# Kernel optimization log

Measured on AMD Instinct MI355X. Metric: run time of the kernel, lower is better.

The kernel has to match this reference:

```python
import jax, jax.numpy as jnp
import numpy as np

B, T, A, FA = 4, 1024, 8, 16   # batch, frames, animals, per-animal feat
C, H, L = 1024, 16, 8          # n_embd, n_head, n_layer
D_IN, D_OUT = A * FA, 256


def _ln(x, g, b, eps=1e-5):
    mu = x.mean(-1, keepdims=True)
    var = ((x - mu) ** 2).mean(-1, keepdims=True)
    return (x - mu) * jax.lax.rsqrt(var + eps) * g + b


def setup_inputs() -> dict:
    key = jax.random.key(0)
    ks = iter(jax.random.split(key, 32))
    w = lambda shape: jax.random.normal(next(ks), shape, jnp.float32) * 0.02
    inp = {
        'tokens': jax.random.normal(next(ks), (B, T, A, FA), jnp.float32),
        'tok_emb_w': w((D_IN, C)), 'tok_emb_b': jnp.zeros((C,), jnp.float32),
        # per-layer params stacked along leading n_layer axis
        'ln1_g': jnp.ones((L, C), jnp.float32), 'ln1_b': jnp.zeros((L, C), jnp.float32),
        'Wq': w((L, C, C)), 'bq': jnp.zeros((L, C), jnp.float32),
        'Wk': w((L, C, C)), 'bk': jnp.zeros((L, C), jnp.float32),
        'Wv': w((L, C, C)), 'bv': jnp.zeros((L, C), jnp.float32),
        'Wo': w((L, C, C)), 'bo': jnp.zeros((L, C), jnp.float32),
        'ln2_g': jnp.ones((L, C), jnp.float32), 'ln2_b': jnp.zeros((L, C), jnp.float32),
        'W1': w((L, C, 4 * C)), 'b1': jnp.zeros((L, 4 * C), jnp.float32),
        'W2': w((L, 4 * C, C)), 'b2': jnp.zeros((L, C), jnp.float32),
        'lnf_g': jnp.ones((C,), jnp.float32), 'lnf_b': jnp.zeros((C,), jnp.float32),
        'proj_w': w((C, D_OUT)), 'proj_b': jnp.zeros((D_OUT,), jnp.float32),
        'dec_w1': w((D_OUT, D_OUT)), 'dec_b1': jnp.zeros((D_OUT,), jnp.float32),
        'dec_ln_g': jnp.ones((D_OUT,), jnp.float32), 'dec_ln_b': jnp.zeros((D_OUT,), jnp.float32),
        'dec_w2': w((D_OUT, D_IN)), 'dec_b2': jnp.zeros((D_IN,), jnp.float32),
    }
    return inp


def reference(tokens, tok_emb_w, tok_emb_b, ln1_g, ln1_b, Wq, bq, Wk, bk, Wv, bv,
              Wo, bo, ln2_g, ln2_b, W1, b1, W2, b2, lnf_g, lnf_b, proj_w, proj_b,
              dec_w1, dec_b1, dec_ln_g, dec_ln_b, dec_w2, dec_b2):
    b, t = tokens.shape[0], tokens.shape[1]
    x = tokens.reshape(b, t, -1)                      # (B,T,D_IN) flatten(2)
    h = x @ tok_emb_w + tok_emb_b                     # (B,T,C)
    mask = jnp.tril(jnp.ones((t, t), bool))           # causal mask
    dh = C // H
    scale = 1.0 / np.sqrt(dh)

    def layer(h, p):
        g1, bb1, wq, bq_, wk, bk_, wv, bv_, wo, bo_, g2, bb2, w1, b1_, w2, b2_ = p
        a = _ln(h, g1, bb1)
        q = (a @ wq + bq_).reshape(b, t, H, dh).transpose(0, 2, 1, 3)
        k = (a @ wk + bk_).reshape(b, t, H, dh).transpose(0, 2, 1, 3)
        v = (a @ wv + bv_).reshape(b, t, H, dh).transpose(0, 2, 1, 3)
        att = jnp.einsum('bhqd,bhkd->bhqk', q, k) * scale
        att = jnp.where(mask, att, -jnp.inf)
        att = jax.nn.softmax(att, axis=-1)
        y = jnp.einsum('bhqk,bhkd->bhqd', att, v)
        y = y.transpose(0, 2, 1, 3).reshape(b, t, C)
        h = h + (y @ wo + bo_)
        m = _ln(h, g2, bb2)
        h = h + jax.nn.gelu(m @ w1 + b1_, approximate=False) @ w2 + b2_
        return h, None

    h, _ = jax.lax.scan(layer, h, (ln1_g, ln1_b, Wq, bq, Wk, bk, Wv, bv, Wo, bo,
                                   ln2_g, ln2_b, W1, b1, W2, b2))
    feats = _ln(h, lnf_g, lnf_b) @ proj_w + proj_b    # (B,T,D_OUT)
    # decode=True path: decoder_frame then frame-delta prediction
    pred = _ln(jnp.tanh(feats @ dec_w1 + dec_b1), dec_ln_g, dec_ln_b) @ dec_w2 + dec_b2
    return pred[:, :-1] - x[:, 1:]                    # (B,T-1,D_IN)
```

## Files before the change

kernel.cpp:

```cpp
#include <hip/hip_runtime.h>
#include <hip/hip_bf16.h>

typedef unsigned short u16;
typedef __attribute__((ext_vector_type(8))) short bf16x8;
typedef __attribute__((ext_vector_type(4))) float f32x4;

#define BT     4096
#define CDIM   1024
#define NH     16
#define FF     4096
#define DIN    128
#define DOUT   256
#define NLAYER 8
#define TSEQ   1024
#define NBATCH 4

__device__ inline u16 f2bfu(float v) {
    __hip_bfloat16 h = __float2bfloat16(v);
    return __builtin_bit_cast(unsigned short, h);
}

__device__ inline void async_copy16(const u16* g, u16* l) {
    __builtin_amdgcn_global_load_lds((const __attribute__((address_space(1))) void*)g,
                                     (__attribute__((address_space(3))) void*)l,
                                     16, 0, 0);
}

template<int ACT, int RES, int OBF, int EPI>
__global__ __launch_bounds__(256) void gemm_bt(
    const u16* __restrict__ A, const u16* __restrict__ Bt,
    const float* __restrict__ bias, const float* res,
    void* outp, u16* __restrict__ vtp, int N, int K, int Kc)
{
    __shared__ __align__(16) u16 As[128 * 32];
    __shared__ __align__(16) u16 Bs[128 * 32];
    int tid  = threadIdx.x;
    int wave = tid >> 6, lane = tid & 63;
    int ln = lane & 15, quad = lane >> 4;
    int wm = (wave >> 1) * 64, wn = (wave & 1) * 64;
    int k0 = blockIdx.z * Kc;
    const u16* Ab = A  + (size_t)blockIdx.y * 128 * K;
    const u16* Bb = Bt + (size_t)blockIdx.x * 128 * K;
    f32x4 acc[4][4] = {};
    for (int kt = k0; kt < k0 + Kc; kt += 32) {
#pragma unroll
        for (int it = 0; it < 2; ++it) {
            int e = it * 256 + tid;
            int row = e >> 2, col = (e & 3) * 8;
            int lbase = (it * 256 + wave * 64) * 8;
            async_copy16(Ab + (size_t)row * K + kt + col, As + lbase);
            async_copy16(Bb + (size_t)row * K + kt + col, Bs + lbase);
        }
        __syncthreads();
        bf16x8 af[4], bfr[4];
#pragma unroll
        for (int i = 0; i < 4; ++i)
            af[i] = *(const bf16x8*)&As[(wm + i * 16 + ln) * 32 + quad * 8];
#pragma unroll
        for (int j = 0; j < 4; ++j)
            bfr[j] = *(const bf16x8*)&Bs[(wn + j * 16 + ln) * 32 + quad * 8];
#pragma unroll
        for (int i = 0; i < 4; ++i)
#pragma unroll
            for (int j = 0; j < 4; ++j)
                acc[i][j] = __builtin_amdgcn_mfma_f32_16x16x32_bf16(af[i], bfr[j], acc[i][j], 0, 0, 0);
        __syncthreads();
    }
    int gr0 = blockIdx.y * 128 + wm + quad * 4;
    int gc0 = blockIdx.x * 128 + wn + ln;
#pragma unroll
    for (int i = 0; i < 4; ++i) {
#pragma unroll
        for (int j = 0; j < 4; ++j) {
            int gc = gc0 + j * 16;
            float bv = (EPI == 1) ? ((blockIdx.z == 0) ? bias[gc] : 0.0f) : bias[gc];
#pragma unroll
            for (int r = 0; r < 4; ++r) {
                int gr = gr0 + i * 16 + r;
                float v = acc[i][j][r] + bv;
                if (ACT == 1) v = 0.5f * v * (1.0f + erff(v * 0.70710678118654752f));
                if (ACT == 2) v = tanhf(v);
                if (EPI == 1) {
                    unsafeAtomicAdd(&((float*)outp)[(size_t)gr * N + gc], v);
                } else if (EPI == 2) {
                    if ((int)blockIdx.x < 16) {
                        ((u16*)outp)[(size_t)gr * 2048 + gc] = f2bfu(v);
                    } else {
                        int c2 = gc - 2048;
                        int hh = c2 >> 6, f = c2 & 63;
                        int bb = gr >> 10, t = gr & 1023;
                        vtp[((size_t)(bb * 16 + hh) * 64 + f) * TSEQ + t] = f2bfu(v);
                    }
                } else {
                    size_t idx = (size_t)gr * N + gc;
                    if (RES) v += res[idx];
                    if (OBF) ((u16*)outp)[idx] = f2bfu(v);
                    else     ((float*)outp)[idx] = v;
                }
            }
        }
    }
}

__global__ __launch_bounds__(64) void attn_kernel(const u16* __restrict__ qk,
    const u16* __restrict__ vT, u16* __restrict__ y)
{
    __shared__ __align__(16) u16 Plds[2][16 * 32];
    int qt = blockIdx.x, bh = blockIdx.y;
    int b = bh >> 4, h = bh & 15;
    int q0 = qt * 32;
    int lane = threadIdx.x;
    int ln = lane & 15, quad = lane >> 4;
    const u16* qbase = qk + (size_t)b * TSEQ * 2048;
    bf16x8 qf[2][2];
#pragma unroll
    for (int qi = 0; qi < 2; ++qi) {
        const u16* qrow = qbase + (size_t)(q0 + qi * 16 + ln) * 2048 + h * 64 + quad * 8;
        qf[qi][0] = *(const bf16x8*)qrow;
        qf[qi][1] = *(const bf16x8*)(qrow + 32);
    }
    const u16* vbase = vT + (size_t)bh * 64 * TSEQ;
    f32x4 O[2][4] = {};
    float m_i[2][4], l_i[2][4];
#pragma unroll
    for (int qi = 0; qi < 2; ++qi)
#pragma unroll
        for (int r = 0; r < 4; ++r) { m_i[qi][r] = -1e30f; l_i[qi][r] = 0.0f; }
    int nkt = qt + 1;
    for (int kt = 0; kt < nkt; ++kt) {
        int j0 = kt * 32;
        bf16x8 kf[2][2];
#pragma unroll
        for (int kk = 0; kk < 2; ++kk) {
            const u16* krow = qbase + (size_t)(j0 + kk * 16 + ln) * 2048 + 1024 + h * 64 + quad * 8;
            kf[kk][0] = *(const bf16x8*)krow;
            kf[kk][1] = *(const bf16x8*)(krow + 32);
        }
        f32x4 S[2][2] = {};
#pragma unroll
        for (int qi = 0; qi < 2; ++qi)
#pragma unroll
            for (int kk = 0; kk < 2; ++kk) {
                S[qi][kk] = __builtin_amdgcn_mfma_f32_16x16x32_bf16(qf[qi][0], kf[kk][0], S[qi][kk], 0, 0, 0);
                S[qi][kk] = __builtin_amdgcn_mfma_f32_16x16x32_bf16(qf[qi][1], kf[kk][1], S[qi][kk], 0, 0, 0);
            }
        bool lastt = (kt == qt);
        float alpha[2][4];
#pragma unroll
        for (int qi = 0; qi < 2; ++qi) {
#pragma unroll
            for (int r = 0; r < 4; ++r) {
                float s0 = S[qi][0][r] * 0.125f, s1 = S[qi][1][r] * 0.125f;
                if (lastt) {
                    int qr = q0 + qi * 16 + quad * 4 + r;
                    if (j0 + ln > qr)      s0 = -1e30f;
                    if (j0 + 16 + ln > qr) s1 = -1e30f;
                }
                float mx = fmaxf(s0, s1);
                mx = fmaxf(mx, __shfl_xor(mx, 1));
                mx = fmaxf(mx, __shfl_xor(mx, 2));
                mx = fmaxf(mx, __shfl_xor(mx, 4));
                mx = fmaxf(mx, __shfl_xor(mx, 8));
                float mn = fmaxf(m_i[qi][r], mx);
                float al = __expf(m_i[qi][r] - mn);
                float p0 = __expf(s0 - mn);
                float p1 = __expf(s1 - mn);
                float rs = p0 + p1;
                rs += __shfl_xor(rs, 1);
                rs += __shfl_xor(rs, 2);
                rs += __shfl_xor(rs, 4);
                rs += __shfl_xor(rs, 8);
                l_i[qi][r] = l_i[qi][r] * al + rs;
                m_i[qi][r] = mn;
                alpha[qi][r] = al;
                Plds[qi][(quad * 4 + r) * 32 + ln]      = f2bfu(p0);
                Plds[qi][(quad * 4 + r) * 32 + 16 + ln] = f2bfu(p1);
            }
#pragma unroll
            for (int nt = 0; nt < 4; ++nt)
#pragma unroll
                for (int r = 0; r < 4; ++r)
                    O[qi][nt][r] *= alpha[qi][r];
        }
        __syncthreads();
        bf16x8 pa0 = *(const bf16x8*)&Plds[0][ln * 32 + quad * 8];
        bf16x8 pa1 = *(const bf16x8*)&Plds[1][ln * 32 + quad * 8];
#pragma unroll
        for (int nt = 0; nt < 4; ++nt) {
            bf16x8 vf = *(const bf16x8*)(vbase + (size_t)(nt * 16 + ln) * TSEQ + j0 + quad * 8);
            O[0][nt] = __builtin_amdgcn_mfma_f32_16x16x32_bf16(pa0, vf, O[0][nt], 0, 0, 0);
            O[1][nt] = __builtin_amdgcn_mfma_f32_16x16x32_bf16(pa1, vf, O[1][nt], 0, 0, 0);
        }
        __syncthreads();
    }
#pragma unroll
    for (int qi = 0; qi < 2; ++qi)
#pragma unroll
        for (int r = 0; r < 4; ++r) {
            float invl = 1.0f / l_i[qi][r];
            int row = q0 + qi * 16 + quad * 4 + r;
#pragma unroll
            for (int nt = 0; nt < 4; ++nt)
                y[(size_t)(b * TSEQ + row) * CDIM + h * 64 + nt * 16 + ln] = f2bfu(O[qi][nt][r] * invl);
        }
}

template<int NPT>
__global__ __launch_bounds__(256) void ln_kernel(const float* __restrict__ x,
    const float* __restrict__ g, const float* __restrict__ bet, u16* __restrict__ out)
{
    const int n = NPT * 256;
    int row = blockIdx.x, tid = threadIdx.x;
    const float* xr = x + (size_t)row * n;
    float xv[NPT];
    float s1 = 0.f, s2 = 0.f;
#pragma unroll
    for (int k = 0; k < NPT; ++k) {
        float v = xr[k * 256 + tid];
        xv[k] = v; s1 += v; s2 += v * v;
    }
#pragma unroll
    for (int m = 1; m < 64; m <<= 1) { s1 += __shfl_xor(s1, m); s2 += __shfl_xor(s2, m); }
    __shared__ float red[8];
    int wv = tid >> 6;
    if ((tid & 63) == 0) { red[wv] = s1; red[4 + wv] = s2; }
    __syncthreads();
    s1 = red[0] + red[1] + red[2] + red[3];
    s2 = red[4] + red[5] + red[6] + red[7];
    float mu = s1 * (1.0f / n);
    float var = s2 * (1.0f / n) - mu * mu;
    float rs = rsqrtf(var + 1e-5f);
#pragma unroll
    for (int k = 0; k < NPT; ++k) {
        int c = k * 256 + tid;
        out[(size_t)row * n + c] = f2bfu((xv[k] - mu) * rs * g[c] + bet[c]);
    }
}

__device__ inline void tile_tc(const float* src, u16* dst, int K, int N, int kt, int nt,
                               int tid, float* sm)
{
    int c = tid & 31, r0 = tid >> 5;
#pragma unroll
    for (int rr = r0; rr < 32; rr += 8)
        sm[rr * 33 + c] = src[(size_t)(kt * 32 + rr) * N + nt * 32 + c];
    __syncthreads();
#pragma unroll
    for (int rr = r0; rr < 32; rr += 8)
        dst[(size_t)(nt * 32 + rr) * K + kt * 32 + c] = f2bfu(sm[c * 33 + rr]);
}

__global__ __launch_bounds__(256) void transpose_cvt(const float* __restrict__ src,
    u16* __restrict__ dst, int K, int N)
{
    __shared__ float sm[32 * 33];
    tile_tc(src, dst, K, N, blockIdx.y, blockIdx.x, threadIdx.x, sm);
}

__global__ __launch_bounds__(256) void prep_layer(
    const float* __restrict__ Wq, const float* __restrict__ Wk, const float* __restrict__ Wv,
    const float* __restrict__ Wo, const float* __restrict__ W1, const float* __restrict__ W2,
    const float* __restrict__ bq, const float* __restrict__ bk, const float* __restrict__ bv,
    u16* __restrict__ qkv_t, u16* __restrict__ wo_t, u16* __restrict__ w1_t,
    u16* __restrict__ w2_t, float* __restrict__ bias3)
{
    __shared__ float sm[32 * 33];
    int id = blockIdx.x, tid = threadIdx.x;
    const float* src; u16* dst; int K, N, kt, nt;
    if (id < 3072) {
        int w = id >> 10, t = id & 1023;
        src = (w == 0) ? Wq : ((w == 1) ? Wk : Wv);
        dst = qkv_t + (size_t)w * CDIM * CDIM;
        K = CDIM; N = CDIM; kt = t >> 5; nt = t & 31;
    } else if (id < 4096) {
        int t = id - 3072; src = Wo; dst = wo_t; K = CDIM; N = CDIM; kt = t >> 5; nt = t & 31;
    } else if (id < 8192) {
        int t = id - 4096; src = W1; dst = w1_t; K = CDIM; N = FF;   kt = t >> 7; nt = t & 127;
    } else {
        int t = id - 8192; src = W2; dst = w2_t; K = FF;   N = CDIM; kt = t >> 5; nt = t & 31;
    }
    tile_tc(src, dst, K, N, kt, nt, tid, sm);
    if (id < 3) {
        const float* bsrc = (id == 0) ? bq : ((id == 1) ? bk : bv);
        for (int k2 = tid; k2 < CDIM; k2 += 256) bias3[id * CDIM + k2] = bsrc[k2];
    }
}

__global__ __launch_bounds__(256) void cvt_bf16(const float* __restrict__ src,
    u16* __restrict__ dst, int n)
{
    int i = blockIdx.x * 256 + threadIdx.x;
    if (i < n) dst[i] = f2bfu(src[i]);
}

__global__ __launch_bounds__(256) void zero_f32(float* __restrict__ dst, int n)
{
    int i = blockIdx.x * 256 + threadIdx.x;
    if (i < n) dst[i] = 0.0f;
}

__global__ __launch_bounds__(256) void out_sub(const float* __restrict__ pred,
    const float* __restrict__ x, float* __restrict__ out, int total)
{
    int i = blockIdx.x * 256 + threadIdx.x;
    if (i >= total) return;
    int b = i / ((TSEQ - 1) * DIN);
    int rtmp = i - b * (TSEQ - 1) * DIN;
    int t = rtmp >> 7, f = rtmp & 127;
    out[i] = pred[(size_t)(b * TSEQ + t) * DIN + f] - x[(size_t)(b * TSEQ + t + 1) * DIN + f];
}

__global__ void fail_flag(float* out) { if (threadIdx.x == 0 && blockIdx.x == 0) out[0] = 1.0e6f; }

extern "C" void kernel_launch(void* const* d_in, const int* in_sizes, int n_in,
                              void* d_out, int out_size, void* d_ws, size_t ws_size,
                              hipStream_t stream)
{
    (void)in_sizes; (void)n_in; (void)out_size;
    const float* tokens    = (const float*)d_in[0];
    const float* tok_emb_w = (const float*)d_in[1];
    const float* tok_emb_b = (const float*)d_in[2];
    const float* ln1_g = (const float*)d_in[3];
    const float* ln1_b = (const float*)d_in[4];
    const float* Wq = (const float*)d_in[5];
    const float* bq = (const float*)d_in[6];
    const float* Wk = (const float*)d_in[7];
    const float* bk = (const float*)d_in[8];
    const float* Wv = (const float*)d_in[9];
    const float* bv = (const float*)d_in[10];
    const float* Wo = (const float*)d_in[11];
    const float* bo = (const float*)d_in[12];
    const float* ln2_g = (const float*)d_in[13];
    const float* ln2_b = (const float*)d_in[14];
    const float* W1 = (const float*)d_in[15];
    const float* b1 = (const float*)d_in[16];
    const float* W2 = (const float*)d_in[17];
    const float* b2 = (const float*)d_in[18];
    const float* lnf_g = (const float*)d_in[19];
    const float* lnf_b = (const float*)d_in[20];
    const float* proj_w = (const float*)d_in[21];
    const float* proj_b = (const float*)d_in[22];
    const float* dec_w1 = (const float*)d_in[23];
    const float* dec_b1 = (const float*)d_in[24];
    const float* dec_ln_g = (const float*)d_in[25];
    const float* dec_ln_b = (const float*)d_in[26];
    const float* dec_w2 = (const float*)d_in[27];
    const float* dec_b2 = (const float*)d_in[28];

    char* p = (char*)d_ws;
    auto alloc = [&](size_t bytes) -> char* {
        char* r = p; p += (bytes + 255) & ~(size_t)255; return r;
    };
    u16*   xb      = (u16*)  alloc((size_t)BT * DIN * 2);
    float* h       = (float*)alloc((size_t)BT * CDIM * 4);
    u16*   abuf    = (u16*)  alloc((size_t)BT * CDIM * 2);
    u16*   qkb     = (u16*)  alloc((size_t)BT * 2048 * 2);
    u16*   vTb     = (u16*)  alloc((size_t)NBATCH * NH * 64 * TSEQ * 2);
    u16*   yb      = (u16*)  alloc((size_t)BT * CDIM * 2);
    u16*   t1      = (u16*)  alloc((size_t)BT * FF * 2);
    u16*   feats   = (u16*)  alloc((size_t)BT * DOUT * 2);
    float* projacc = (float*)alloc((size_t)BT * DOUT * 4);
    float* d1      = (float*)alloc((size_t)BT * DOUT * 4);
    u16*   d1n     = (u16*)  alloc((size_t)BT * DOUT * 2);
    float* pred    = (float*)alloc((size_t)BT * DIN * 4);
    u16*   emb_t   = (u16*)  alloc((size_t)CDIM * DIN * 2);
    u16*   proj_t  = (u16*)  alloc((size_t)DOUT * CDIM * 2);
    u16*   dec1_t  = (u16*)  alloc((size_t)DOUT * DOUT * 2);
    u16*   dec2_t  = (u16*)  alloc((size_t)DIN * DOUT * 2);
    u16*   qkv_t   = (u16*)  alloc((size_t)3 * CDIM * CDIM * 2);
    u16*   wo_t    = (u16*)  alloc((size_t)CDIM * CDIM * 2);
    u16*   w1_t    = (u16*)  alloc((size_t)FF * CDIM * 2);
    u16*   w2_t    = (u16*)  alloc((size_t)CDIM * FF * 2);
    float* bias3   = (float*)alloc((size_t)3 * CDIM * 4);
    if ((size_t)(p - (char*)d_ws) > ws_size) {
        fail_flag<<<1, 64, 0, stream>>>((float*)d_out);
        return;
    }

    cvt_bf16<<<(BT * DIN) / 256, 256, 0, stream>>>(tokens, xb, BT * DIN);
    transpose_cvt<<<dim3(CDIM / 32, DIN / 32),  256, 0, stream>>>(tok_emb_w, emb_t,  DIN,  CDIM);
    transpose_cvt<<<dim3(DOUT / 32, CDIM / 32), 256, 0, stream>>>(proj_w,    proj_t, CDIM, DOUT);
    transpose_cvt<<<dim3(DOUT / 32, DOUT / 32), 256, 0, stream>>>(dec_w1,    dec1_t, DOUT, DOUT);
    transpose_cvt<<<dim3(DIN / 32,  DOUT / 32), 256, 0, stream>>>(dec_w2,    dec2_t, DOUT, DIN);
    gemm_bt<0, 0, 0, 0><<<dim3(CDIM / 128, BT / 128, 1), 256, 0, stream>>>(
        xb, emb_t, tok_emb_b, nullptr, h, nullptr, CDIM, DIN, DIN);

    for (int l = 0; l < NLAYER; ++l) {
        prep_layer<<<12288, 256, 0, stream>>>(
            Wq + (size_t)l * CDIM * CDIM, Wk + (size_t)l * CDIM * CDIM,
            Wv + (size_t)l * CDIM * CDIM, Wo + (size_t)l * CDIM * CDIM,
            W1 + (size_t)l * CDIM * FF,   W2 + (size_t)l * FF * CDIM,
            bq + l * CDIM, bk + l * CDIM, bv + l * CDIM,
            qkv_t, wo_t, w1_t, w2_t, bias3);
        ln_kernel<4><<<BT, 256, 0, stream>>>(h, ln1_g + l * CDIM, ln1_b + l * CDIM, abuf);
        gemm_bt<0, 0, 1, 2><<<dim3(3 * CDIM / 128, BT / 128, 1), 256, 0, stream>>>(
            abuf, qkv_t, bias3, nullptr, qkb, vTb, 3 * CDIM, CDIM, CDIM);
        attn_kernel<<<dim3(TSEQ / 32, NBATCH * NH), 64, 0, stream>>>(qkb, vTb, yb);
        gemm_bt<0, 0, 0, 1><<<dim3(CDIM / 128, BT / 128, 2), 256, 0, stream>>>(
            yb, wo_t, bo + l * CDIM, nullptr, h, nullptr, CDIM, CDIM, CDIM / 2);
        ln_kernel<4><<<BT, 256, 0, stream>>>(h, ln2_g + l * CDIM, ln2_b + l * CDIM, abuf);
        gemm_bt<1, 0, 1, 0><<<dim3(FF / 128, BT / 128, 1), 256, 0, stream>>>(
            abuf, w1_t, b1 + l * FF, nullptr, t1, nullptr, FF, CDIM, CDIM);
        gemm_bt<0, 0, 0, 1><<<dim3(CDIM / 128, BT / 128, 2), 256, 0, stream>>>(
            t1, w2_t, b2 + l * CDIM, nullptr, h, nullptr, CDIM, FF, FF / 2);
    }

    ln_kernel<4><<<BT, 256, 0, stream>>>(h, lnf_g, lnf_b, abuf);
    zero_f32<<<(BT * DOUT) / 256, 256, 0, stream>>>(projacc, BT * DOUT);
    gemm_bt<0, 0, 0, 1><<<dim3(DOUT / 128, BT / 128, 4), 256, 0, stream>>>(
        abuf, proj_t, proj_b, nullptr, projacc, nullptr, DOUT, CDIM, CDIM / 4);
    cvt_bf16<<<(BT * DOUT) / 256, 256, 0, stream>>>(projacc, feats, BT * DOUT);
    gemm_bt<2, 0, 0, 0><<<dim3(DOUT / 128, BT / 128, 1), 256, 0, stream>>>(
        feats, dec1_t, dec_b1, nullptr, d1, nullptr, DOUT, DOUT, DOUT);
    ln_kernel<1><<<BT, 256, 0, stream>>>(d1, dec_ln_g, dec_ln_b, d1n);
    gemm_bt<0, 0, 0, 0><<<dim3(DIN / 128, BT / 128, 1), 256, 0, stream>>>(
        d1n, dec2_t, dec_b2, nullptr, pred, nullptr, DIN, DOUT, DOUT);
    int total = NBATCH * (TSEQ - 1) * DIN;
    out_sub<<<(total + 255) / 256, 256, 0, stream>>>(pred, tokens, (float*)d_out, total);
}
```

Before: 3.137 ms.

## Split attention key loop across four waves with LDS softmax merge

The attention kernel now runs four waves per block, each handling every fourth key tile, and the partial outputs, maxima and sums are combined through shared memory in a flash-decoding style merge. Blocks are remapped so the longest causal query tiles are scheduled first. This targets low per-block parallelism and load imbalance from the causal triangle, and removes the per-tile block barriers. In exchange it adds shared-memory traffic, a final reduction step and higher LDS usage per block.

```diff
diff --git a/kernel.cpp b/kernel.cpp
--- a/kernel.cpp
+++ b/kernel.cpp
@@ -102,15 +102,22 @@
     }
 }
 
-__global__ __launch_bounds__(64) void attn_kernel(const u16* __restrict__ qk,
+__global__ __launch_bounds__(256) void attn_kernel(const u16* __restrict__ qk,
     const u16* __restrict__ vT, u16* __restrict__ y)
 {
-    __shared__ __align__(16) u16 Plds[2][16 * 32];
-    int qt = blockIdx.x, bh = blockIdx.y;
+    __shared__ __align__(16) float Osm[4][32][64];
+    __shared__ float msm[4][32], lsm[4][32];
+    int id = blockIdx.x;
+    int bh = (id & 7) + 8 * ((id >> 3) & 7);
+    int qt = 31 - (id >> 6);
     int b = bh >> 4, h = bh & 15;
     int q0 = qt * 32;
-    int lane = threadIdx.x;
+    int tid = threadIdx.x;
+    int wave = tid >> 6, lane = tid & 63;
     int ln = lane & 15, quad = lane >> 4;
+    u16* P0 = (u16*)&Osm[wave][0][0];
+    u16* P1 = P0 + 512;
+
     const u16* qbase = qk + (size_t)b * TSEQ * 2048;
     bf16x8 qf[2][2];
 #pragma unroll
@@ -126,8 +133,9 @@
     for (int qi = 0; qi < 2; ++qi)
 #pragma unroll
         for (int r = 0; r < 4; ++r) { m_i[qi][r] = -1e30f; l_i[qi][r] = 0.0f; }
+
     int nkt = qt + 1;
-    for (int kt = 0; kt < nkt; ++kt) {
+    for (int kt = wave; kt < nkt; kt += 4) {
         int j0 = kt * 32;
         bf16x8 kf[2][2];
 #pragma unroll
@@ -173,8 +181,9 @@
                 l_i[qi][r] = l_i[qi][r] * al + rs;
                 m_i[qi][r] = mn;
                 alpha[qi][r] = al;
-                Plds[qi][(quad * 4 + r) * 32 + ln]      = f2bfu(p0);
-                Plds[qi][(quad * 4 + r) * 32 + 16 + ln] = f2bfu(p1);
+                u16* Pq = qi ? P1 : P0;
+                Pq[(quad * 4 + r) * 32 + ln]      = f2bfu(p0);
+                Pq[(quad * 4 + r) * 32 + 16 + ln] = f2bfu(p1);
             }
 #pragma unroll
             for (int nt = 0; nt < 4; ++nt)
@@ -182,27 +191,42 @@
                 for (int r = 0; r < 4; ++r)
                     O[qi][nt][r] *= alpha[qi][r];
         }
-        __syncthreads();
-        bf16x8 pa0 = *(const bf16x8*)&Plds[0][ln * 32 + quad * 8];
-        bf16x8 pa1 = *(const bf16x8*)&Plds[1][ln * 32 + quad * 8];
+        bf16x8 pa0 = *(const bf16x8*)&P0[ln * 32 + quad * 8];
+        bf16x8 pa1 = *(const bf16x8*)&P1[ln * 32 + quad * 8];
 #pragma unroll
         for (int nt = 0; nt < 4; ++nt) {
             bf16x8 vf = *(const bf16x8*)(vbase + (size_t)(nt * 16 + ln) * TSEQ + j0 + quad * 8);
             O[0][nt] = __builtin_amdgcn_mfma_f32_16x16x32_bf16(pa0, vf, O[0][nt], 0, 0, 0);
             O[1][nt] = __builtin_amdgcn_mfma_f32_16x16x32_bf16(pa1, vf, O[1][nt], 0, 0, 0);
         }
-        __syncthreads();
     }
 #pragma unroll
     for (int qi = 0; qi < 2; ++qi)
 #pragma unroll
         for (int r = 0; r < 4; ++r) {
-            float invl = 1.0f / l_i[qi][r];
-            int row = q0 + qi * 16 + quad * 4 + r;
+            int row = qi * 16 + quad * 4 + r;
+            if (ln == 0) { msm[wave][row] = m_i[qi][r]; lsm[wave][row] = l_i[qi][r]; }
 #pragma unroll
             for (int nt = 0; nt < 4; ++nt)
-                y[(size_t)(b * TSEQ + row) * CDIM + h * 64 + nt * 16 + ln] = f2bfu(O[qi][nt][r] * invl);
-        }
+                Osm[wave][row][nt * 16 + ln] = O[qi][nt][r];
+        }
+    __syncthreads();
+    {
+        int row = tid >> 3;
+        int c0 = (tid & 7) * 8;
+        float m0 = msm[0][row], m1 = msm[1][row], m2 = msm[2][row], m3 = msm[3][row];
+        float ms = fmaxf(fmaxf(m0, m1), fmaxf(m2, m3));
+        float e0 = __expf(m0 - ms), e1 = __expf(m1 - ms), e2 = __expf(m2 - ms), e3 = __expf(m3 - ms);
+        float ls = lsm[0][row] * e0 + lsm[1][row] * e1 + lsm[2][row] * e2 + lsm[3][row] * e3;
+        float inv = 1.0f / ls;
+        u16* yr = y + (size_t)(b * TSEQ + q0 + row) * CDIM + h * 64 + c0;
+#pragma unroll
+        for (int j = 0; j < 8; ++j) {
+            float o = Osm[0][row][c0 + j] * e0 + Osm[1][row][c0 + j] * e1
+                    + Osm[2][row][c0 + j] * e2 + Osm[3][row][c0 + j] * e3;
+            yr[j] = f2bfu(o * inv);
+        }
+    }
 }
 
 template<int NPT>
@@ -395,7 +419,7 @@
         ln_kernel<4><<<BT, 256, 0, stream>>>(h, ln1_g + l * CDIM, ln1_b + l * CDIM, abuf);
         gemm_bt<0, 0, 1, 2><<<dim3(3 * CDIM / 128, BT / 128, 1), 256, 0, stream>>>(
             abuf, qkv_t, bias3, nullptr, qkb, vTb, 3 * CDIM, CDIM, CDIM);
-        attn_kernel<<<dim3(TSEQ / 32, NBATCH * NH), 64, 0, stream>>>(qkb, vTb, yb);
+        attn_kernel<<<2048, 256, 0, stream>>>(qkb, vTb, yb);
         gemm_bt<0, 0, 0, 1><<<dim3(CDIM / 128, BT / 128, 2), 256, 0, stream>>>(
             yb, wo_t, bo + l * CDIM, nullptr, h, nullptr, CDIM, CDIM, CDIM / 2);
         ln_kernel<4><<<BT, 256, 0, stream>>>(h, ln2_g + l * CDIM, ln2_b + l * CDIM, abuf);
```

Result: faster. 2.843 ms (-9.4%).
